# Optimization experiments

Hardware: AMD Instinct MI355X
Metric: run time of the kernel (lower is better)

Reference implementation:

```python
import jax, jax.numpy as jnp
import numpy as np

LOCAL_RADIUS = 84
MAX_REL_DIST = 12
USE_HARD_G2L = True
USE_HARD_L2G = True


def _rel_id(rel, max_d):
    # clip relative position and map to id: 0..max_d for >=0, max_d+1..2*max_d for <0
    rel = jnp.clip(rel, -max_d, max_d)
    return jnp.where(rel >= 0, rel, max_d - rel)


def setup_inputs() -> dict:
    key = jax.random.key(0)
    k1, k2, k3 = jax.random.split(key, 3)
    B, L, G = 16, 4096, 256
    long_bp = jax.random.randint(k1, (B, L), 0, 2, dtype=jnp.int32)
    long_pid = jnp.sort(jax.random.randint(k2, (B, L), 0, G, dtype=jnp.int32), axis=-1)
    glob_bp = jax.random.randint(k3, (B, G), 0, 2, dtype=jnp.int32)
    return {
        'long_paragraph_breakpoints': long_bp,
        'long_paragraph_ids': long_pid,
        'global_paragraph_breakpoints': glob_bp,
    }


def reference(long_paragraph_breakpoints, long_paragraph_ids, global_paragraph_breakpoints):
    B, L = long_paragraph_breakpoints.shape
    G = global_paragraph_breakpoints.shape[1]
    R = LOCAL_RADIUS
    D = MAX_REL_DIST
    vocab = 2 * D + 1  # relative_vocab_size

    # reverse cumsum -> segment ids (distinct paragraph segments counted from the end)
    long_seg = jnp.cumsum(long_paragraph_breakpoints[:, ::-1], axis=-1)[:, ::-1]
    glob_seg = jnp.cumsum(global_paragraph_breakpoints[:, ::-1], axis=-1)[:, ::-1]

    # l2l: local segmented attention mask, window of 2R+1 around each token
    pad_seg = jnp.pad(long_seg, ((0, 0), (R, R)), constant_values=-1)
    win_idx = jnp.arange(L)[:, None] + jnp.arange(2 * R + 1)[None, :]  # [L, 2R+1]
    win = pad_seg[:, win_idx]  # [B, L, 2R+1]
    l2l_att_mask = (win == long_seg[:, :, None]).astype(jnp.int32)

    # input masks from breakpoint segments
    long_tokens = jnp.minimum(1, long_seg)
    glob_tokens = jnp.minimum(1, glob_seg)

    g2g_att_mask = (glob_tokens[:, :, None] == glob_tokens[:, None, :]).astype(jnp.int32)
    l2g_att_mask = (long_tokens[:, :, None] == glob_tokens[:, None, :]).astype(jnp.int32)
    g2l_att_mask = jnp.transpose(l2g_att_mask, (0, 2, 1))

    grange = jnp.arange(G, dtype=long_paragraph_ids.dtype)
    if USE_HARD_G2L:
        hard_g2l = (grange[None, :, None] == long_paragraph_ids[:, None, :]) | (grange[None, :, None] == 0)
        g2l_att_mask = g2l_att_mask * hard_g2l.astype(jnp.int32)
    if USE_HARD_L2G:
        hard_l2g = (long_paragraph_ids[:, :, None] == grange[None, None, :])
        l2g_att_mask = l2g_att_mask * hard_l2g.astype(jnp.int32)

    # l2l relative ids: constant per window offset
    offs = jnp.arange(-R, R + 1)
    l2l_rel = jnp.broadcast_to(_rel_id(offs, D).astype(jnp.int32)[None, None, :], (B, L, 2 * R + 1))

    # l2g / g2l relative ids: paragraph-match indicator shifted past the rel vocab
    l2g_rel = (grange[None, None, :] == long_paragraph_ids[:, :, None]).astype(jnp.int32)
    g2l_rel = jnp.transpose(l2g_rel, (0, 2, 1)) + vocab
    l2g_rel = l2g_rel + vocab

    # g2g relative ids with cross-segment positions overwritten
    rel = jnp.arange(G)[None, :] - jnp.arange(G)[:, None]
    g2g_rel = _rel_id(rel, D).astype(jnp.int32)  # [G, G]
    same_seg = glob_seg[:, :, None] == glob_seg[:, None, :]
    g2g_rel = jnp.where(same_seg, g2g_rel[None, :, :], jnp.int32(vocab + 2))

    return (l2l_att_mask, g2g_att_mask, l2g_att_mask, g2l_att_mask,
            l2l_rel, g2g_rel, l2g_rel, g2l_rel)
```

## Files before the change

### kernel.cpp

```cpp
#include <hip/hip_runtime.h>

#define BB 16
#define LL 4096
#define GG 256
#define RR 84
#define WW 169
#define DD 12
#define VOCAB 25

#define S_L2L (BB * LL * WW)
#define S_G2G (BB * GG * GG)
#define S_L2G (BB * LL * GG)
#define S_G2L (BB * GG * LL)
#define OFF0 0
#define OFF1 (OFF0 + S_L2L)
#define OFF2 (OFF1 + S_G2G)
#define OFF3 (OFF2 + S_L2G)
#define OFF4 (OFF3 + S_G2L)
#define OFF5 (OFF4 + S_L2L)
#define OFF6 (OFF5 + S_G2G)
#define OFF7 (OFF6 + S_L2G)

#define NB_L2L (S_L2L / 1024)
#define NB_G2G (S_G2G / 1024)
#define NB_L2G (S_L2G / 1024)
#define NB_G2L (S_G2L / 1024)
#define NB_TOTAL (NB_L2L + NB_G2G + NB_L2G + NB_G2L)

__global__ void scan_kernel(const int* __restrict__ long_bp,
                            const int* __restrict__ glob_bp,
                            int* __restrict__ long_seg,
                            int* __restrict__ glob_seg) {
    const int b = blockIdx.x;
    const int t = threadIdx.x;
    __shared__ int part[256];

    const int* bp = long_bp + b * LL;
    int vals[16];
    int s = 0;
#pragma unroll
    for (int j = 0; j < 16; ++j) { vals[j] = bp[t * 16 + j]; s += vals[j]; }
    part[t] = s;
    __syncthreads();
    for (int off = 1; off < 256; off <<= 1) {
        int v = (t >= off) ? part[t - off] : 0;
        __syncthreads();
        part[t] += v;
        __syncthreads();
    }
    const int total = part[255];
    int run = (t == 0) ? 0 : part[t - 1];
    int* seg = long_seg + b * LL;
#pragma unroll
    for (int j = 0; j < 16; ++j) {
        seg[t * 16 + j] = total - run;
        run += vals[j];
    }
    __syncthreads();

    const int gv = glob_bp[b * GG + t];
    part[t] = gv;
    __syncthreads();
    for (int off = 1; off < 256; off <<= 1) {
        int v = (t >= off) ? part[t - off] : 0;
        __syncthreads();
        part[t] += v;
        __syncthreads();
    }
    const int gtot = part[255];
    const int gexcl = (t == 0) ? 0 : part[t - 1];
    glob_seg[b * GG + t] = gtot - gexcl;
}

__global__ __launch_bounds__(256) void fused_writer(
        const int* __restrict__ long_seg,
        const int* __restrict__ long_pid,
        const int* __restrict__ glob_seg,
        int* __restrict__ out) {
    const int blk = blockIdx.x;
    const int tid = threadIdx.x;

    if (blk < NB_L2L) {
        unsigned f = (unsigned)blk * 1024u + (unsigned)tid * 4u;
        unsigned row = f / (unsigned)WW;
        int k = (int)(f - row * (unsigned)WW);
        int i = (int)(row & (LL - 1));
        unsigned base = row - (unsigned)i;
        int segi = long_seg[row];
        int m[4], r[4];
#pragma unroll
        for (int e = 0; e < 4; ++e) {
            const int j = i + k - RR;
            int msk = 0;
            if (j >= 0 && j < LL) msk = (long_seg[base + (unsigned)j] == segi) ? 1 : 0;
            int c = k - RR;
            c = c < -DD ? -DD : (c > DD ? DD : c);
            r[e] = (c >= 0) ? c : (DD - c);
            m[e] = msk;
            if (e < 3) {
                if (++k == WW) {
                    k = 0; ++row;
                    i = (int)(row & (LL - 1));
                    base = row - (unsigned)i;
                    segi = long_seg[row];
                }
            }
        }
        *(int4*)(out + OFF0 + f) = make_int4(m[0], m[1], m[2], m[3]);
        *(int4*)(out + OFF4 + f) = make_int4(r[0], r[1], r[2], r[3]);

    } else if (blk < NB_L2L + NB_G2G) {
        const int blk2 = blk - NB_L2L;
        const unsigned f = (unsigned)blk2 * 1024u + (unsigned)tid * 4u;
        const int h0 = (int)(f & (GG - 1));
        const unsigned row = f >> 8;
        const int g = (int)(row & (GG - 1));
        const int segg = glob_seg[row];
        const int tokg = segg > 0 ? 1 : 0;
        const int4 sh = *(const int4*)(glob_seg + (row - (unsigned)g) + (unsigned)h0);
        const int sgh[4] = {sh.x, sh.y, sh.z, sh.w};
        int m[4], r[4];
#pragma unroll
        for (int e = 0; e < 4; ++e) {
            const int tokh = sgh[e] > 0 ? 1 : 0;
            int c = (h0 + e) - g;
            c = c < -DD ? -DD : (c > DD ? DD : c);
            const int r0 = (c >= 0) ? c : (DD - c);
            m[e] = (tokg == tokh) ? 1 : 0;
            r[e] = (segg == sgh[e]) ? r0 : (VOCAB + 2);
        }
        *(int4*)(out + OFF1 + f) = make_int4(m[0], m[1], m[2], m[3]);
        *(int4*)(out + OFF5 + f) = make_int4(r[0], r[1], r[2], r[3]);

    } else if (blk < NB_L2L + NB_G2G + NB_L2G) {
        const int blk3 = blk - (NB_L2L + NB_G2G);
        const unsigned f = (unsigned)blk3 * 1024u + (unsigned)tid * 4u;
        const int g0 = (int)(f & (GG - 1));
        const unsigned row = f >> 8;
        const int b = (int)(row >> 12);
        const int tokl = long_seg[row] > 0 ? 1 : 0;
        const int pid = long_pid[row];
        const int4 sg = *(const int4*)(glob_seg + b * GG + g0);
        const int sgv[4] = {sg.x, sg.y, sg.z, sg.w};
        int m[4], r[4];
#pragma unroll
        for (int e = 0; e < 4; ++e) {
            const int tokg = sgv[e] > 0 ? 1 : 0;
            const int eq = (pid == (g0 + e)) ? 1 : 0;
            m[e] = (tokl == tokg) ? eq : 0;
            r[e] = eq + VOCAB;
        }
        *(int4*)(out + OFF2 + f) = make_int4(m[0], m[1], m[2], m[3]);
        *(int4*)(out + OFF6 + f) = make_int4(r[0], r[1], r[2], r[3]);

    } else {
        const int blk4 = blk - (NB_L2L + NB_G2G + NB_L2G);
        const unsigned f = (unsigned)blk4 * 1024u + (unsigned)tid * 4u;
        const int i0 = (int)(f & (LL - 1));
        const unsigned row = f >> 12;
        const int g = (int)(row & (GG - 1));
        const int b = (int)(row >> 8);
        const int tokg = glob_seg[row] > 0 ? 1 : 0;
        const int4 pid4 = *(const int4*)(long_pid + b * LL + i0);
        const int4 seg4 = *(const int4*)(long_seg + b * LL + i0);
        const int pidv[4] = {pid4.x, pid4.y, pid4.z, pid4.w};
        const int segv[4] = {seg4.x, seg4.y, seg4.z, seg4.w};
        const int gz = (g == 0) ? 1 : 0;
        int m[4], r[4];
#pragma unroll
        for (int e = 0; e < 4; ++e) {
            const int tokl = segv[e] > 0 ? 1 : 0;
            const int eq = (g == pidv[e]) ? 1 : 0;
            const int allow = eq | gz;
            m[e] = (tokl == tokg) ? allow : 0;
            r[e] = eq + VOCAB;
        }
        *(int4*)(out + OFF3 + f) = make_int4(m[0], m[1], m[2], m[3]);
        *(int4*)(out + OFF7 + f) = make_int4(r[0], r[1], r[2], r[3]);
    }
}

extern "C" void kernel_launch(void* const* d_in, const int* in_sizes, int n_in,
                              void* d_out, int out_size, void* d_ws, size_t ws_size,
                              hipStream_t stream) {
    const int* long_bp  = (const int*)d_in[0];
    const int* long_pid = (const int*)d_in[1];
    const int* glob_bp  = (const int*)d_in[2];
    int* out = (int*)d_out;

    int* long_seg = (int*)d_ws;
    int* glob_seg = long_seg + BB * LL;

    scan_kernel<<<BB, 256, 0, stream>>>(long_bp, glob_bp, long_seg, glob_seg);
    fused_writer<<<NB_TOTAL, 256, 0, stream>>>(long_seg, long_pid, glob_seg, out);
}
```

Measured before the change: 358.5 us.

## Precompute per-row segment limits, widen per-thread work, use nontemporal stores

The scan kernel now runs binary searches over the sorted segment row to compute each token's same-segment window bounds. The l2l writer then builds its mask from a range comparison instead of gathering neighbour segment ids. All writer branches now handle 8 elements per thread and use nontemporal vector stores, to cut gather loads and cache pollution on this write-bound kernel. The cost is extra serial work in the scan kernel, which runs only 16 blocks, plus a small extra workspace array.

```diff
diff --git a/kernel.cpp b/kernel.cpp
--- a/kernel.cpp
+++ b/kernel.cpp
@@ -21,19 +21,28 @@
 #define OFF6 (OFF5 + S_G2G)
 #define OFF7 (OFF6 + S_L2G)
 
-#define NB_L2L (S_L2L / 1024)
-#define NB_G2G (S_G2G / 1024)
-#define NB_L2G (S_L2G / 1024)
-#define NB_G2L (S_G2L / 1024)
+#define NB_L2L (S_L2L / 2048)
+#define NB_G2G (S_G2G / 2048)
+#define NB_L2G (S_L2G / 2048)
+#define NB_G2L (S_G2L / 2048)
 #define NB_TOTAL (NB_L2L + NB_G2G + NB_L2G + NB_G2L)
+
+typedef int v4i __attribute__((ext_vector_type(4)));
+
+static __device__ __forceinline__ void st_nt(int* p, int a, int b, int c, int d) {
+    v4i v = {a, b, c, d};
+    __builtin_nontemporal_store(v, (v4i*)p);
+}
 
 __global__ void scan_kernel(const int* __restrict__ long_bp,
                             const int* __restrict__ glob_bp,
                             int* __restrict__ long_seg,
-                            int* __restrict__ glob_seg) {
+                            int* __restrict__ glob_seg,
+                            int2* __restrict__ lims) {
     const int b = blockIdx.x;
     const int t = threadIdx.x;
     __shared__ int part[256];
+    __shared__ int srow[LL];
 
     const int* bp = long_bp + b * LL;
     int vals[16];
@@ -53,8 +62,24 @@
     int* seg = long_seg + b * LL;
 #pragma unroll
     for (int j = 0; j < 16; ++j) {
-        seg[t * 16 + j] = total - run;
+        const int v = total - run;
+        seg[t * 16 + j] = v;
+        srow[t * 16 + j] = v;
         run += vals[j];
+    }
+    __syncthreads();
+
+#pragma unroll 1
+    for (int j = 0; j < 16; ++j) {
+        const int i = t * 16 + j;
+        const int v = srow[i];
+        int l = 0, h = i;
+        while (l < h) { const int mid = (l + h) >> 1; if (srow[mid] <= v) h = mid; else l = mid + 1; }
+        const int lo = l;
+        l = i + 1; h = LL;
+        while (l < h) { const int mid = (l + h) >> 1; if (srow[mid] < v) h = mid; else l = mid + 1; }
+        const int hi = l - 1;
+        lims[b * LL + i] = make_int2(lo - i + RR, hi - i + RR);
     }
     __syncthreads();
 
@@ -70,113 +95,128 @@
     const int gtot = part[255];
     const int gexcl = (t == 0) ? 0 : part[t - 1];
     glob_seg[b * GG + t] = gtot - gexcl;
+}
+
+static __device__ __forceinline__ int rel_of_k(int k) {
+    int c = k - RR;
+    c = c < -DD ? -DD : (c > DD ? DD : c);
+    return (c >= 0) ? c : (DD - c);
 }
 
 __global__ __launch_bounds__(256) void fused_writer(
         const int* __restrict__ long_seg,
         const int* __restrict__ long_pid,
         const int* __restrict__ glob_seg,
+        const int2* __restrict__ lims,
         int* __restrict__ out) {
     const int blk = blockIdx.x;
     const int tid = threadIdx.x;
 
     if (blk < NB_L2L) {
-        unsigned f = (unsigned)blk * 1024u + (unsigned)tid * 4u;
-        unsigned row = f / (unsigned)WW;
-        int k = (int)(f - row * (unsigned)WW);
-        int i = (int)(row & (LL - 1));
-        unsigned base = row - (unsigned)i;
-        int segi = long_seg[row];
-        int m[4], r[4];
-#pragma unroll
-        for (int e = 0; e < 4; ++e) {
-            const int j = i + k - RR;
-            int msk = 0;
-            if (j >= 0 && j < LL) msk = (long_seg[base + (unsigned)j] == segi) ? 1 : 0;
-            int c = k - RR;
-            c = c < -DD ? -DD : (c > DD ? DD : c);
-            r[e] = (c >= 0) ? c : (DD - c);
-            m[e] = msk;
-            if (e < 3) {
-                if (++k == WW) {
-                    k = 0; ++row;
-                    i = (int)(row & (LL - 1));
-                    base = row - (unsigned)i;
-                    segi = long_seg[row];
-                }
+        const unsigned f = ((unsigned)blk * 256u + (unsigned)tid) * 8u;
+        const unsigned row0 = f / (unsigned)WW;
+        const int k0 = (int)(f - row0 * (unsigned)WW);
+        int m[8], r[8];
+        if (k0 <= WW - 8) {
+            const int2 lm = lims[row0];
+#pragma unroll
+            for (int e = 0; e < 8; ++e) {
+                const int ke = k0 + e;
+                m[e] = (ke >= lm.x && ke <= lm.y) ? 1 : 0;
+                r[e] = rel_of_k(ke);
             }
-        }
-        *(int4*)(out + OFF0 + f) = make_int4(m[0], m[1], m[2], m[3]);
-        *(int4*)(out + OFF4 + f) = make_int4(r[0], r[1], r[2], r[3]);
+        } else {
+#pragma unroll
+            for (int e = 0; e < 8; ++e) {
+                const unsigned fe = f + (unsigned)e;
+                const unsigned rowe = fe / (unsigned)WW;
+                const int ke = (int)(fe - rowe * (unsigned)WW);
+                const int2 lm = lims[rowe];
+                m[e] = (ke >= lm.x && ke <= lm.y) ? 1 : 0;
+                r[e] = rel_of_k(ke);
+            }
+        }
+        st_nt(out + OFF0 + f,     m[0], m[1], m[2], m[3]);
+        st_nt(out + OFF0 + f + 4, m[4], m[5], m[6], m[7]);
+        st_nt(out + OFF4 + f,     r[0], r[1], r[2], r[3]);
+        st_nt(out + OFF4 + f + 4, r[4], r[5], r[6], r[7]);
 
     } else if (blk < NB_L2L + NB_G2G) {
-        const int blk2 = blk - NB_L2L;
-        const unsigned f = (unsigned)blk2 * 1024u + (unsigned)tid * 4u;
+        const unsigned f = ((unsigned)(blk - NB_L2L) * 256u + (unsigned)tid) * 8u;
+        const unsigned row = f >> 8;
         const int h0 = (int)(f & (GG - 1));
-        const unsigned row = f >> 8;
         const int g = (int)(row & (GG - 1));
         const int segg = glob_seg[row];
         const int tokg = segg > 0 ? 1 : 0;
-        const int4 sh = *(const int4*)(glob_seg + (row - (unsigned)g) + (unsigned)h0);
-        const int sgh[4] = {sh.x, sh.y, sh.z, sh.w};
-        int m[4], r[4];
-#pragma unroll
-        for (int e = 0; e < 4; ++e) {
-            const int tokh = sgh[e] > 0 ? 1 : 0;
-            int c = (h0 + e) - g;
-            c = c < -DD ? -DD : (c > DD ? DD : c);
-            const int r0 = (c >= 0) ? c : (DD - c);
+        const int* hp = glob_seg + (row - (unsigned)g) + (unsigned)h0;
+        const int4 sa = *(const int4*)hp;
+        const int4 sb = *(const int4*)(hp + 4);
+        const int sh[8] = {sa.x, sa.y, sa.z, sa.w, sb.x, sb.y, sb.z, sb.w};
+        int m[8], r[8];
+#pragma unroll
+        for (int e = 0; e < 8; ++e) {
+            const int tokh = sh[e] > 0 ? 1 : 0;
             m[e] = (tokg == tokh) ? 1 : 0;
-            r[e] = (segg == sgh[e]) ? r0 : (VOCAB + 2);
-        }
-        *(int4*)(out + OFF1 + f) = make_int4(m[0], m[1], m[2], m[3]);
-        *(int4*)(out + OFF5 + f) = make_int4(r[0], r[1], r[2], r[3]);
+            r[e] = (segg == sh[e]) ? rel_of_k(h0 + e - g + RR) : (VOCAB + 2);
+        }
+        st_nt(out + OFF1 + f,     m[0], m[1], m[2], m[3]);
+        st_nt(out + OFF1 + f + 4, m[4], m[5], m[6], m[7]);
+        st_nt(out + OFF5 + f,     r[0], r[1], r[2], r[3]);
+        st_nt(out + OFF5 + f + 4, r[4], r[5], r[6], r[7]);
 
     } else if (blk < NB_L2L + NB_G2G + NB_L2G) {
-        const int blk3 = blk - (NB_L2L + NB_G2G);
-        const unsigned f = (unsigned)blk3 * 1024u + (unsigned)tid * 4u;
+        const unsigned f = ((unsigned)(blk - NB_L2L - NB_G2G) * 256u + (unsigned)tid) * 8u;
+        const unsigned row = f >> 8;
         const int g0 = (int)(f & (GG - 1));
-        const unsigned row = f >> 8;
         const int b = (int)(row >> 12);
         const int tokl = long_seg[row] > 0 ? 1 : 0;
         const int pid = long_pid[row];
-        const int4 sg = *(const int4*)(glob_seg + b * GG + g0);
-        const int sgv[4] = {sg.x, sg.y, sg.z, sg.w};
-        int m[4], r[4];
-#pragma unroll
-        for (int e = 0; e < 4; ++e) {
-            const int tokg = sgv[e] > 0 ? 1 : 0;
+        const int* gp = glob_seg + b * GG + g0;
+        const int4 sa = *(const int4*)gp;
+        const int4 sb = *(const int4*)(gp + 4);
+        const int sg[8] = {sa.x, sa.y, sa.z, sa.w, sb.x, sb.y, sb.z, sb.w};
+        int m[8], r[8];
+#pragma unroll
+        for (int e = 0; e < 8; ++e) {
+            const int tokg = sg[e] > 0 ? 1 : 0;
             const int eq = (pid == (g0 + e)) ? 1 : 0;
             m[e] = (tokl == tokg) ? eq : 0;
             r[e] = eq + VOCAB;
         }
-        *(int4*)(out + OFF2 + f) = make_int4(m[0], m[1], m[2], m[3]);
-        *(int4*)(out + OFF6 + f) = make_int4(r[0], r[1], r[2], r[3]);
+        st_nt(out + OFF2 + f,     m[0], m[1], m[2], m[3]);
+        st_nt(out + OFF2 + f + 4, m[4], m[5], m[6], m[7]);
+        st_nt(out + OFF6 + f,     r[0], r[1], r[2], r[3]);
+        st_nt(out + OFF6 + f + 4, r[4], r[5], r[6], r[7]);
 
     } else {
-        const int blk4 = blk - (NB_L2L + NB_G2G + NB_L2G);
-        const unsigned f = (unsigned)blk4 * 1024u + (unsigned)tid * 4u;
+        const unsigned f = ((unsigned)(blk - NB_L2L - NB_G2G - NB_L2G) * 256u + (unsigned)tid) * 8u;
+        const unsigned row = f >> 12;
         const int i0 = (int)(f & (LL - 1));
-        const unsigned row = f >> 12;
         const int g = (int)(row & (GG - 1));
         const int b = (int)(row >> 8);
         const int tokg = glob_seg[row] > 0 ? 1 : 0;
-        const int4 pid4 = *(const int4*)(long_pid + b * LL + i0);
-        const int4 seg4 = *(const int4*)(long_seg + b * LL + i0);
-        const int pidv[4] = {pid4.x, pid4.y, pid4.z, pid4.w};
-        const int segv[4] = {seg4.x, seg4.y, seg4.z, seg4.w};
         const int gz = (g == 0) ? 1 : 0;
-        int m[4], r[4];
-#pragma unroll
-        for (int e = 0; e < 4; ++e) {
-            const int tokl = segv[e] > 0 ? 1 : 0;
-            const int eq = (g == pidv[e]) ? 1 : 0;
+        const int* pp = long_pid + b * LL + i0;
+        const int* sp = long_seg + b * LL + i0;
+        const int4 p0 = *(const int4*)pp;
+        const int4 p1 = *(const int4*)(pp + 4);
+        const int4 s0 = *(const int4*)sp;
+        const int4 s1 = *(const int4*)(sp + 4);
+        const int pv[8] = {p0.x, p0.y, p0.z, p0.w, p1.x, p1.y, p1.z, p1.w};
+        const int sv[8] = {s0.x, s0.y, s0.z, s0.w, s1.x, s1.y, s1.z, s1.w};
+        int m[8], r[8];
+#pragma unroll
+        for (int e = 0; e < 8; ++e) {
+            const int tokl = sv[e] > 0 ? 1 : 0;
+            const int eq = (g == pv[e]) ? 1 : 0;
             const int allow = eq | gz;
             m[e] = (tokl == tokg) ? allow : 0;
             r[e] = eq + VOCAB;
         }
-        *(int4*)(out + OFF3 + f) = make_int4(m[0], m[1], m[2], m[3]);
-        *(int4*)(out + OFF7 + f) = make_int4(r[0], r[1], r[2], r[3]);
+        st_nt(out + OFF3 + f,     m[0], m[1], m[2], m[3]);
+        st_nt(out + OFF3 + f + 4, m[4], m[5], m[6], m[7]);
+        st_nt(out + OFF7 + f,     r[0], r[1], r[2], r[3]);
+        st_nt(out + OFF7 + f + 4, r[4], r[5], r[6], r[7]);
     }
 }
 
@@ -188,9 +228,10 @@
     const int* glob_bp  = (const int*)d_in[2];
     int* out = (int*)d_out;
 
-    int* long_seg = (int*)d_ws;
-    int* glob_seg = long_seg + BB * LL;
-
-    scan_kernel<<<BB, 256, 0, stream>>>(long_bp, glob_bp, long_seg, glob_seg);
-    fused_writer<<<NB_TOTAL, 256, 0, stream>>>(long_seg, long_pid, glob_seg, out);
-}
+    int*  long_seg = (int*)d_ws;
+    int*  glob_seg = long_seg + BB * LL;
+    int2* lims     = (int2*)(glob_seg + BB * GG);
+
+    scan_kernel<<<BB, 256, 0, stream>>>(long_bp, glob_bp, long_seg, glob_seg, lims);
+    fused_writer<<<NB_TOTAL, 256, 0, stream>>>(long_seg, long_pid, glob_seg, lims, out);
+}
```

Result: slower. 476.2 us (+32.8%).
